# Kernel tuning notes

Hardware: AMD Instinct MI355X
Metric: run time of the kernel (lower is better)

The kernel has to match this reference:

```python
import jax, jax.numpy as jnp
import numpy as np

N_SEGMENT = 8  # frames per clip
N_DIV = 8      # fold divisor: fold = C // N_DIV channels shift each way


def setup_inputs() -> dict:
    key = jax.random.key(0)
    k1, k2 = jax.random.split(key)
    x = jax.random.normal(k1, (128, 256, 28, 28), dtype=jnp.float32)  # [nt, C, H, W], nt = 16 clips * 8 frames
    net_weight = jax.random.normal(k2, (256, 256), dtype=jnp.float32) * 0.0625  # 1x1 conv [out_c, in_c]
    return {"x": x, "net_weight": net_weight}


def temporal_shift(x):
    # x: [nt, C, H, W]. Equivalent to the fixed one-hot depthwise Conv3d (k=3, pad=1):
    #   channels [:fold]        -> out[t] = x[t-1]  (weight[...,0]=1)
    #   channels [fold:2*fold]  -> out[t] = x[t+1]  (weight[...,2]=1)
    #   channels [2*fold:]      -> out[t] = x[t]    (weight[...,1]=1)
    nt, c, h, w = x.shape
    b = nt // N_SEGMENT
    xv = x.reshape(b, N_SEGMENT, c, h, w)
    fold = c // N_DIV
    prev = jnp.pad(xv[:, :-1, :fold], ((0, 0), (1, 0), (0, 0), (0, 0), (0, 0)))       # shift right in time
    nxt = jnp.pad(xv[:, 1:, fold:2 * fold], ((0, 0), (0, 1), (0, 0), (0, 0), (0, 0)))  # shift left in time
    shifted = jnp.concatenate([prev, nxt, xv[:, :, 2 * fold:]], axis=2)
    return shifted.reshape(nt, c, h, w)


def reference(x, net_weight):
    y = temporal_shift(x)
    # wrapped net: 1x1 Conv2d(256 -> 256, bias=False) == per-pixel GEMM
    out = jnp.einsum('nchw,oc->nohw', y, net_weight)
    return out
```

## Files before the change

kernel.cpp:

```cpp
#include <hip/hip_runtime.h>
#include <hip/hip_bf16.h>


#define CDIM 256
#define HWPX 784
#define FRST (CDIM * HWPX)
#define P_TILE 112
#define NPT  7
#define NWG  (128 * NPT * 2)
#define LROW 264

using bf16x8 = __attribute__((ext_vector_type(8))) short;
using bf16x4 = __attribute__((ext_vector_type(4))) short;
using f32x4  = __attribute__((ext_vector_type(4))) float;

static __device__ __forceinline__ unsigned int pk2(float lo, float hi) {
    union { __hip_bfloat162 h; unsigned int u; } cv;
    cv.h = __float22bfloat162_rn(make_float2(lo, hi));
    return cv.u;
}

__global__ void wconv(const float* __restrict__ w, unsigned short* __restrict__ wb) {
    const int i = (blockIdx.x * 256 + threadIdx.x) * 4;
    f32x4 v = *(const f32x4*)(w + i);
    *(uint2*)(wb + i) = make_uint2(pk2(v[0], v[1]), pk2(v[2], v[3]));
}

__global__ __launch_bounds__(256, 2)
void tsm_ksplit(const float* __restrict__ x,
                const unsigned short* __restrict__ wb,
                float* __restrict__ out) {
    __shared__ __align__(16) unsigned short y[P_TILE * LROW];

    const int bid = blockIdx.x;
    const int wg  = (bid & 7) * (NWG / 8) + (bid >> 3);
    const int h    = wg & 1;
    const int pair = wg >> 1;
    const int n    = pair / NPT;
    const int pt   = pair - n * NPT;
    const int p0   = pt * P_TILE;
    const int tid  = threadIdx.x;
    const int tf   = n & 7;

    const int lane = tid & 63;
    const int wv   = tid >> 6;
    const int g    = lane >> 4;
    const int ol   = lane & 15;

    bf16x8 wf[8][2];
    #pragma unroll
    for (int kk = 0; kk < 8; ++kk)
        #pragma unroll
        for (int m = 0; m < 2; ++m) {
            const unsigned short* wp =
                &wb[(size_t)(h * 128 + wv * 32 + m * 16 + ol) * CDIM + kk * 32 + g * 8];
            asm volatile("global_load_dwordx4 %0, %1, off"
                         : "=v"(wf[kk][m]) : "v"(wp));
        }

    f32x4 r0[14], r1[14];
    #pragma unroll
    for (int i = 0; i < 14; ++i) {
        const int idx = tid + i * 256;
        const int cp  = idx / 28;
        const int pv  = idx - cp * 28;
        const int c0  = cp * 2;
        const int d   = (cp < 16) ? -1 : (cp < 32 ? 1 : 0);
        const bool valid = !((d == -1 && tf == 0) || (d == 1 && tf == 7));
        const float* s = x + ((size_t)(n + (valid ? d : 0)) * CDIM + c0) * HWPX
                           + p0 + pv * 4;
        asm volatile("global_load_dwordx4 %0, %1, off" : "=v"(r0[i]) : "v"(s));
        const float* s1 = s + HWPX;
        asm volatile("global_load_dwordx4 %0, %1, off" : "=v"(r1[i]) : "v"(s1));
    }

    #define WRITE_ITEM(i)                                                      \
    {                                                                          \
        const int idx = tid + (i) * 256;                                       \
        const int cp  = idx / 28;                                              \
        const int pv  = idx - cp * 28;                                         \
        const int c0  = cp * 2;                                                \
        const int d   = (cp < 16) ? -1 : (cp < 32 ? 1 : 0);                    \
        const bool valid = !((d == -1 && tf == 0) || (d == 1 && tf == 7));     \
        const int cc  = c0 ^ (((pv >> 1) & 7) << 2);       \
        const int rb  = pv * 4 * LROW + cc;                                    \
        _Pragma("unroll")                                                      \
        for (int r = 0; r < 4; ++r)                                            \
            *(unsigned int*)&y[rb + r * LROW] =                                \
                valid ? pk2(r0[i][r], r1[i][r]) : 0u;                          \
    }

    asm volatile("s_waitcnt vmcnt(14)" ::: "memory");
    __builtin_amdgcn_sched_barrier(0);
    #pragma unroll
    for (int i = 0; i < 7; ++i) WRITE_ITEM(i)
    __syncthreads();

    f32x4 acc[2][7];
    #pragma unroll
    for (int m = 0; m < 2; ++m)
        #pragma unroll
        for (int nn = 0; nn < 7; ++nn)
            acc[m][nn] = f32x4{0.f, 0.f, 0.f, 0.f};

    #define COMPUTE(K0, K1)                                                    \
    {                                                                          \
        _Pragma("unroll")                                                      \
        for (int nn = 0; nn < 7; ++nn) {                                       \
            const int p    = nn * 16 + ol;                                     \
            const int zz   = ((p >> 3) & 7) << 2;                              \
            const int rowb = p * LROW;                                         \
            _Pragma("unroll")                                                  \
            for (int kk = (K0); kk < (K1); ++kk) {                             \
                const int c  = kk * 32 + g * 8;                                \
                const int e0 = c ^ zz;                                         \
                const bf16x4 lo = *(const bf16x4*)&y[rowb + e0];               \
                const bf16x4 hi = *(const bf16x4*)&y[rowb + (e0 ^ 4)];         \
                const bf16x8 bf = __builtin_shufflevector(lo, hi,              \
                                                          0, 1, 2, 3, 4, 5, 6, 7); \
                acc[0][nn] = __builtin_amdgcn_mfma_f32_16x16x32_bf16(          \
                    wf[kk][0], bf, acc[0][nn], 0, 0, 0);                       \
                acc[1][nn] = __builtin_amdgcn_mfma_f32_16x16x32_bf16(          \
                    wf[kk][1], bf, acc[1][nn], 0, 0, 0);                       \
            }                                                                  \
        }                                                                      \
    }

    COMPUTE(0, 4)

    asm volatile("s_waitcnt vmcnt(0)" ::: "memory");
    __builtin_amdgcn_sched_barrier(0);
    #pragma unroll
    for (int i = 7; i < 14; ++i) WRITE_ITEM(i)
    __syncthreads();

    COMPUTE(4, 8)

    const size_t outbase = (size_t)n * CDIM * HWPX + p0 + ol;
    #pragma unroll
    for (int m = 0; m < 2; ++m) {
        #pragma unroll
        for (int r = 0; r < 4; ++r) {
            const int o = h * 128 + wv * 32 + m * 16 + g * 4 + r;
            float* orow = out + outbase + (size_t)o * HWPX;
            #pragma unroll
            for (int nn = 0; nn < 7; ++nn)
                orow[nn * 16] = acc[m][nn][r];
        }
    }
    #undef WRITE_ITEM
    #undef COMPUTE
}

#define LDS_STRIDE 264
__global__ __launch_bounds__(512, 4)
void tsm_fallback(const float* __restrict__ x, const float* __restrict__ w,
                  float* __restrict__ out) {
    __shared__ __align__(16) unsigned short ylds[P_TILE * LDS_STRIDE];
    const int n = blockIdx.x, tile = blockIdx.y, p0 = tile * P_TILE;
    const int tid = threadIdx.x, tf = n & 7;
    f32x4 v0[7], v1[7]; int cps[7], pvs[7];
    #pragma unroll
    for (int i = 0; i < 7; ++i) {
        const int idx = tid + i * 512, cp = idx / 28, pv = idx - cp * 28;
        cps[i] = cp; pvs[i] = pv;
        const int c0 = cp * 2;
        int nsrc; bool valid;
        if (c0 < 32)      { nsrc = n - 1; valid = (tf > 0); }
        else if (c0 < 64) { nsrc = n + 1; valid = (tf < 7); }
        else              { nsrc = n;     valid = true; }
        const float* src = x + ((size_t)(valid ? nsrc : n) * CDIM + c0) * HWPX + p0 + pv * 4;
        f32x4 a = {0,0,0,0}, b = {0,0,0,0};
        if (valid) { a = *(const f32x4*)src; b = *(const f32x4*)(src + HWPX); }
        v0[i] = a; v1[i] = b;
    }
    #pragma unroll
    for (int i = 0; i < 7; ++i) {
        const int c0 = cps[i] * 2, pv = pvs[i];
        const int cc = c0 ^ ((pv & 7) << 3);
        const int rb = pv * 4 * LDS_STRIDE + cc;
        #pragma unroll
        for (int r = 0; r < 4; ++r)
            *(unsigned int*)&ylds[rb + r * LDS_STRIDE] = pk2(v0[i][r], v1[i][r]);
    }
    __syncthreads();
    const int lane = tid & 63, wv = tid >> 6, g = lane >> 4, ol = lane & 15;
    f32x4 acc[2][7];
    #pragma unroll
    for (int m = 0; m < 2; ++m)
        #pragma unroll
        for (int nn = 0; nn < 7; ++nn) acc[m][nn] = f32x4{0,0,0,0};
    #pragma unroll
    for (int kk = 0; kk < 8; ++kk) {
        const int c = kk * 32 + g * 8;
        bf16x8 af[2];
        #pragma unroll
        for (int m = 0; m < 2; ++m) {
            const float* wp = w + (size_t)(wv * 32 + m * 16 + ol) * CDIM + c;
            f32x4 w0 = *(const f32x4*)wp, w1 = *(const f32x4*)(wp + 4);
            union { bf16x8 v; unsigned int u4[4]; } cv;
            cv.u4[0] = pk2(w0[0], w0[1]); cv.u4[1] = pk2(w0[2], w0[3]);
            cv.u4[2] = pk2(w1[0], w1[1]); cv.u4[3] = pk2(w1[2], w1[3]);
            af[m] = cv.v;
        }
        #pragma unroll
        for (int nn = 0; nn < 7; ++nn) {
            const int p = nn * 16 + ol;
            const int cc = c ^ (((p >> 2) & 7) << 3);
            const bf16x8 bf = *(const bf16x8*)&ylds[p * LDS_STRIDE + cc];
            #pragma unroll
            for (int m = 0; m < 2; ++m)
                acc[m][nn] = __builtin_amdgcn_mfma_f32_16x16x32_bf16(af[m], bf, acc[m][nn], 0, 0, 0);
        }
    }
    const size_t outbase = (size_t)n * CDIM * HWPX + p0 + ol;
    #pragma unroll
    for (int m = 0; m < 2; ++m)
        #pragma unroll
        for (int r = 0; r < 4; ++r) {
            const int o = wv * 32 + m * 16 + g * 4 + r;
            float* orow = out + outbase + (size_t)o * HWPX;
            #pragma unroll
            for (int nn = 0; nn < 7; ++nn) orow[nn * 16] = acc[m][nn][r];
        }
}

extern "C" void kernel_launch(void* const* d_in, const int* in_sizes, int n_in,
                              void* d_out, int out_size, void* d_ws, size_t ws_size,
                              hipStream_t stream) {
    const float* x = (const float*)d_in[0];
    const float* w = (const float*)d_in[1];
    float* out     = (float*)d_out;
    const size_t wb_bytes = (size_t)CDIM * CDIM * sizeof(unsigned short);
    if (ws_size >= wb_bytes) {
        unsigned short* wbuf = (unsigned short*)d_ws;
        wconv<<<64, 256, 0, stream>>>(w, wbuf);
        tsm_ksplit<<<NWG, 256, 0, stream>>>(x, wbuf, out);
    } else {
        tsm_fallback<<<dim3(128, 7, 1), dim3(512, 1, 1), 0, stream>>>(x, w, out);
    }
}
```

Before: 48.59 us.

## Process two frames per workgroup and prefetch the second frame during compute

Each workgroup now handles frame n1 and frame n1+64, which share the same temporal position and therefore the same shift pattern. The grid is halved. The bf16 weight fragments held in registers are reused across both frames, and the second frame's input loads are issued while the first frame's MFMAs and output stores run. The aim is to amortise the weight loads and launch cost and to hide global load latency. The costs are more register pressure, a longer per-workgroup critical path, and fewer workgroups (1.75 waves), which may worsen tail balance on an already bandwidth-heavy kernel.

```diff
diff --git a/kernel.cpp b/kernel.cpp
--- a/kernel.cpp
+++ b/kernel.cpp
@@ -7,7 +7,7 @@
 #define FRST (CDIM * HWPX)
 #define P_TILE 112
 #define NPT  7
-#define NWG  (128 * NPT * 2)
+#define NWGB 896
 #define LROW 264
 
 using bf16x8 = __attribute__((ext_vector_type(8))) short;
@@ -27,20 +27,21 @@
 }
 
 __global__ __launch_bounds__(256, 2)
-void tsm_ksplit(const float* __restrict__ x,
-                const unsigned short* __restrict__ wb,
-                float* __restrict__ out) {
+void tsm_pair(const float* __restrict__ x,
+              const unsigned short* __restrict__ wb,
+              float* __restrict__ out) {
     __shared__ __align__(16) unsigned short y[P_TILE * LROW];
 
-    const int bid = blockIdx.x;
-    const int wg  = (bid & 7) * (NWG / 8) + (bid >> 3);
+    const int bid  = blockIdx.x;
+    const int wg   = (bid & 7) * (NWGB / 8) + (bid >> 3);
     const int h    = wg & 1;
     const int pair = wg >> 1;
-    const int n    = pair / NPT;
-    const int pt   = pair - n * NPT;
+    const int n1   = pair / NPT;
+    const int pt   = pair - n1 * NPT;
     const int p0   = pt * P_TILE;
+    const int n2   = n1 + 64;
     const int tid  = threadIdx.x;
-    const int tf   = n & 7;
+    const int tf   = n1 & 7;
 
     const int lane = tid & 63;
     const int wv   = tid >> 6;
@@ -59,19 +60,21 @@
         }
 
     f32x4 r0[14], r1[14];
-    #pragma unroll
-    for (int i = 0; i < 14; ++i) {
-        const int idx = tid + i * 256;
-        const int cp  = idx / 28;
-        const int pv  = idx - cp * 28;
-        const int c0  = cp * 2;
-        const int d   = (cp < 16) ? -1 : (cp < 32 ? 1 : 0);
-        const bool valid = !((d == -1 && tf == 0) || (d == 1 && tf == 7));
-        const float* s = x + ((size_t)(n + (valid ? d : 0)) * CDIM + c0) * HWPX
-                           + p0 + pv * 4;
-        asm volatile("global_load_dwordx4 %0, %1, off" : "=v"(r0[i]) : "v"(s));
-        const float* s1 = s + HWPX;
-        asm volatile("global_load_dwordx4 %0, %1, off" : "=v"(r1[i]) : "v"(s1));
+    f32x4 acc[2][7];
+
+    #define ISSUE(i, N_)                                                       \
+    {                                                                          \
+        const int idx = tid + (i) * 256;                                       \
+        const int cp  = idx / 28;                                              \
+        const int pv  = idx - cp * 28;                                         \
+        const int c0  = cp * 2;                                                \
+        const int d   = (cp < 16) ? -1 : (cp < 32 ? 1 : 0);                    \
+        const bool valid = !((d == -1 && tf == 0) || (d == 1 && tf == 7));     \
+        const float* s = x + ((size_t)((N_) + (valid ? d : 0)) * CDIM + c0) * HWPX \
+                           + p0 + pv * 4;                                      \
+        asm volatile("global_load_dwordx4 %0, %1, off" : "=v"(r0[i]) : "v"(s));\
+        const float* s1 = s + HWPX;                                            \
+        asm volatile("global_load_dwordx4 %0, %1, off" : "=v"(r1[i]) : "v"(s1));\
     }
 
     #define WRITE_ITEM(i)                                                      \
@@ -90,18 +93,14 @@
                 valid ? pk2(r0[i][r], r1[i][r]) : 0u;                          \
     }
 
-    asm volatile("s_waitcnt vmcnt(14)" ::: "memory");
-    __builtin_amdgcn_sched_barrier(0);
-    #pragma unroll
-    for (int i = 0; i < 7; ++i) WRITE_ITEM(i)
-    __syncthreads();
-
-    f32x4 acc[2][7];
-    #pragma unroll
-    for (int m = 0; m < 2; ++m)
-        #pragma unroll
-        for (int nn = 0; nn < 7; ++nn)
-            acc[m][nn] = f32x4{0.f, 0.f, 0.f, 0.f};
+    #define ZERO_ACC                                                           \
+    {                                                                          \
+        _Pragma("unroll")                                                      \
+        for (int m = 0; m < 2; ++m)                                            \
+            _Pragma("unroll")                                                  \
+            for (int nn = 0; nn < 7; ++nn)                                     \
+                acc[m][nn] = f32x4{0.f, 0.f, 0.f, 0.f};                        \
+    }
 
     #define COMPUTE(K0, K1)                                                    \
     {                                                                          \
@@ -126,6 +125,32 @@
         }                                                                      \
     }
 
+    #define STORES(N_)                                                         \
+    {                                                                          \
+        const size_t outbase = (size_t)(N_) * CDIM * HWPX + p0 + ol;           \
+        _Pragma("unroll")                                                      \
+        for (int m = 0; m < 2; ++m) {                                          \
+            _Pragma("unroll")                                                  \
+            for (int r = 0; r < 4; ++r) {                                      \
+                const int o = h * 128 + wv * 32 + m * 16 + g * 4 + r;          \
+                float* orow = out + outbase + (size_t)o * HWPX;                \
+                _Pragma("unroll")                                              \
+                for (int nn = 0; nn < 7; ++nn)                                 \
+                    orow[nn * 16] = acc[m][nn][r];                             \
+            }                                                                  \
+        }                                                                      \
+    }
+
+    #pragma unroll
+    for (int i = 0; i < 14; ++i) ISSUE(i, n1)
+
+    asm volatile("s_waitcnt vmcnt(14)" ::: "memory");
+    __builtin_amdgcn_sched_barrier(0);
+    #pragma unroll
+    for (int i = 0; i < 7; ++i) WRITE_ITEM(i)
+    __syncthreads();
+
+    ZERO_ACC
     COMPUTE(0, 4)
 
     asm volatile("s_waitcnt vmcnt(0)" ::: "memory");
@@ -134,22 +159,37 @@
     for (int i = 7; i < 14; ++i) WRITE_ITEM(i)
     __syncthreads();
 
+    #pragma unroll
+    for (int i = 0; i < 7; ++i) ISSUE(i, n2)
     COMPUTE(4, 8)
-
-    const size_t outbase = (size_t)n * CDIM * HWPX + p0 + ol;
-    #pragma unroll
-    for (int m = 0; m < 2; ++m) {
-        #pragma unroll
-        for (int r = 0; r < 4; ++r) {
-            const int o = h * 128 + wv * 32 + m * 16 + g * 4 + r;
-            float* orow = out + outbase + (size_t)o * HWPX;
-            #pragma unroll
-            for (int nn = 0; nn < 7; ++nn)
-                orow[nn * 16] = acc[m][nn][r];
-        }
-    }
+    STORES(n1)
+
+    __syncthreads();
+    asm volatile("s_waitcnt vmcnt(56)" ::: "memory");
+    __builtin_amdgcn_sched_barrier(0);
+    #pragma unroll
+    for (int i = 0; i < 7; ++i) WRITE_ITEM(i)
+    __syncthreads();
+
+    ZERO_ACC
+    #pragma unroll
+    for (int i = 7; i < 14; ++i) ISSUE(i, n2)
+    COMPUTE(0, 4)
+
+    asm volatile("s_waitcnt vmcnt(0)" ::: "memory");
+    __builtin_amdgcn_sched_barrier(0);
+    #pragma unroll
+    for (int i = 7; i < 14; ++i) WRITE_ITEM(i)
+    __syncthreads();
+
+    COMPUTE(4, 8)
+    STORES(n2)
+
+    #undef ISSUE
     #undef WRITE_ITEM
+    #undef ZERO_ACC
     #undef COMPUTE
+    #undef STORES
 }
 
 #define LDS_STRIDE 264
@@ -235,7 +275,7 @@
     if (ws_size >= wb_bytes) {
         unsigned short* wbuf = (unsigned short*)d_ws;
         wconv<<<64, 256, 0, stream>>>(w, wbuf);
-        tsm_ksplit<<<NWG, 256, 0, stream>>>(x, wbuf, out);
+        tsm_pair<<<NWGB, 256, 0, stream>>>(x, wbuf, out);
     } else {
         tsm_fallback<<<dim3(128, 7, 1), dim3(512, 1, 1), 0, stream>>>(x, w, out);
     }
```

Result: slower. 102.8 us (+111.7%).

## Replace output-half split with full-output 64-pixel tiles and streamed weights

Applied to the files above, without the earlier changes.

Each workgroup now computes all 256 output channels for a flat 64-pixel tile that may cross frame boundaries, instead of half the outputs for a 112-pixel tile. Before, every input tile was loaded and converted twice, once per output half. Now each input is read once, and the weights are streamed in two K passes of 16 registers each. The cost is more weight-load traffic per pixel, smaller tiles, and per-element frame index division.

```diff
diff --git a/kernel.cpp b/kernel.cpp
--- a/kernel.cpp
+++ b/kernel.cpp
@@ -5,9 +5,8 @@
 #define CDIM 256
 #define HWPX 784
 #define FRST (CDIM * HWPX)
-#define P_TILE 112
-#define NPT  7
-#define NWG  (128 * NPT * 2)
+#define TPX  64
+#define NTILES 1568
 #define LROW 264
 
 using bf16x8 = __attribute__((ext_vector_type(8))) short;
@@ -27,60 +26,65 @@
 }
 
 __global__ __launch_bounds__(256, 2)
-void tsm_ksplit(const float* __restrict__ x,
-                const unsigned short* __restrict__ wb,
-                float* __restrict__ out) {
-    __shared__ __align__(16) unsigned short y[P_TILE * LROW];
+void tsm_full(const float* __restrict__ x,
+              const unsigned short* __restrict__ wb,
+              float* __restrict__ out) {
+    __shared__ __align__(16) unsigned short y[TPX * LROW];
 
     const int bid = blockIdx.x;
-    const int wg  = (bid & 7) * (NWG / 8) + (bid >> 3);
-    const int h    = wg & 1;
-    const int pair = wg >> 1;
-    const int n    = pair / NPT;
-    const int pt   = pair - n * NPT;
-    const int p0   = pt * P_TILE;
-    const int tid  = threadIdx.x;
-    const int tf   = n & 7;
-
+    const int t   = (bid & 7) * (NTILES / 8) + (bid >> 3);
+    const int tid = threadIdx.x;
     const int lane = tid & 63;
     const int wv   = tid >> 6;
     const int g    = lane >> 4;
     const int ol   = lane & 15;
 
-    bf16x8 wf[8][2];
-    #pragma unroll
-    for (int kk = 0; kk < 8; ++kk)
-        #pragma unroll
-        for (int m = 0; m < 2; ++m) {
-            const unsigned short* wp =
-                &wb[(size_t)(h * 128 + wv * 32 + m * 16 + ol) * CDIM + kk * 32 + g * 8];
-            asm volatile("global_load_dwordx4 %0, %1, off"
-                         : "=v"(wf[kk][m]) : "v"(wp));
-        }
-
-    f32x4 r0[14], r1[14];
-    #pragma unroll
-    for (int i = 0; i < 14; ++i) {
-        const int idx = tid + i * 256;
-        const int cp  = idx / 28;
-        const int pv  = idx - cp * 28;
-        const int c0  = cp * 2;
-        const int d   = (cp < 16) ? -1 : (cp < 32 ? 1 : 0);
-        const bool valid = !((d == -1 && tf == 0) || (d == 1 && tf == 7));
-        const float* s = x + ((size_t)(n + (valid ? d : 0)) * CDIM + c0) * HWPX
-                           + p0 + pv * 4;
-        asm volatile("global_load_dwordx4 %0, %1, off" : "=v"(r0[i]) : "v"(s));
-        const float* s1 = s + HWPX;
-        asm volatile("global_load_dwordx4 %0, %1, off" : "=v"(r1[i]) : "v"(s1));
-    }
-
-    #define WRITE_ITEM(i)                                                      \
+    bf16x8 wf[4][4];
+    f32x4  r0[8], r1[8];
+    f32x4  acc[4][4];
+
+    #define WISSUE(PASS)                                                       \
+    {                                                                          \
+        _Pragma("unroll")                                                      \
+        for (int kkh = 0; kkh < 4; ++kkh)                                      \
+            _Pragma("unroll")                                                  \
+            for (int m = 0; m < 4; ++m) {                                      \
+                const unsigned short* wp_ = wb +                               \
+                    (size_t)(wv * 64 + m * 16 + ol) * CDIM +                   \
+                    ((PASS) * 4 + kkh) * 32 + g * 8;                           \
+                asm volatile("global_load_dwordx4 %0, %1, off"                 \
+                             : "=v"(wf[kkh][m]) : "v"(wp_));                   \
+            }                                                                  \
+    }
+
+    #define ISSUE(i)                                                           \
     {                                                                          \
         const int idx = tid + (i) * 256;                                       \
-        const int cp  = idx / 28;                                              \
-        const int pv  = idx - cp * 28;                                         \
+        const int cp  = idx >> 4;                                              \
+        const int pv  = idx & 15;                                              \
         const int c0  = cp * 2;                                                \
         const int d   = (cp < 16) ? -1 : (cp < 32 ? 1 : 0);                    \
+        const int gq  = t * TPX + pv * 4;                                      \
+        const int nf  = gq / HWPX;                                             \
+        const int pin = gq - nf * HWPX;                                        \
+        const int tf  = nf & 7;                                                \
+        const bool valid = !((d == -1 && tf == 0) || (d == 1 && tf == 7));     \
+        const float* s = x + ((size_t)(nf + (valid ? d : 0)) * CDIM + c0) * HWPX + pin; \
+        asm volatile("global_load_dwordx4 %0, %1, off" : "=v"(r0[i]) : "v"(s));\
+        const float* s1 = s + HWPX;                                            \
+        asm volatile("global_load_dwordx4 %0, %1, off" : "=v"(r1[i]) : "v"(s1));\
+    }
+
+    #define WRITE_ITEM(i)                                                      \
+    {                                                                          \
+        const int idx = tid + (i) * 256;                                       \
+        const int cp  = idx >> 4;                                              \
+        const int pv  = idx & 15;                                              \
+        const int c0  = cp * 2;                                                \
+        const int d   = (cp < 16) ? -1 : (cp < 32 ? 1 : 0);                    \
+        const int gq  = t * TPX + pv * 4;                                      \
+        const int nf  = gq / HWPX;                                             \
+        const int tf  = nf & 7;                                                \
         const bool valid = !((d == -1 && tf == 0) || (d == 1 && tf == 7));     \
         const int cc  = c0 ^ (((pv >> 1) & 7) << 2);       \
         const int rb  = pv * 4 * LROW + cc;                                    \
@@ -90,68 +94,79 @@
                 valid ? pk2(r0[i][r], r1[i][r]) : 0u;                          \
     }
 
-    asm volatile("s_waitcnt vmcnt(14)" ::: "memory");
-    __builtin_amdgcn_sched_barrier(0);
-    #pragma unroll
-    for (int i = 0; i < 7; ++i) WRITE_ITEM(i)
-    __syncthreads();
-
-    f32x4 acc[2][7];
-    #pragma unroll
-    for (int m = 0; m < 2; ++m)
-        #pragma unroll
-        for (int nn = 0; nn < 7; ++nn)
-            acc[m][nn] = f32x4{0.f, 0.f, 0.f, 0.f};
-
-    #define COMPUTE(K0, K1)                                                    \
+    #define COMPUTE(PASS)                                                      \
     {                                                                          \
         _Pragma("unroll")                                                      \
-        for (int nn = 0; nn < 7; ++nn) {                                       \
-            const int p    = nn * 16 + ol;                                     \
-            const int zz   = ((p >> 3) & 7) << 2;                              \
-            const int rowb = p * LROW;                                         \
+        for (int nn = 0; nn < 4; ++nn) {                                       \
+            const int lp   = nn * 16 + ol;                                     \
+            const int zz   = ((lp >> 3) & 7) << 2;                             \
+            const int rowb = lp * LROW;                                        \
             _Pragma("unroll")                                                  \
-            for (int kk = (K0); kk < (K1); ++kk) {                             \
-                const int c  = kk * 32 + g * 8;                                \
+            for (int kkh = 0; kkh < 4; ++kkh) {                                \
+                const int c  = ((PASS) * 4 + kkh) * 32 + g * 8;                \
                 const int e0 = c ^ zz;                                         \
                 const bf16x4 lo = *(const bf16x4*)&y[rowb + e0];               \
                 const bf16x4 hi = *(const bf16x4*)&y[rowb + (e0 ^ 4)];         \
                 const bf16x8 bf = __builtin_shufflevector(lo, hi,              \
                                                           0, 1, 2, 3, 4, 5, 6, 7); \
-                acc[0][nn] = __builtin_amdgcn_mfma_f32_16x16x32_bf16(          \
-                    wf[kk][0], bf, acc[0][nn], 0, 0, 0);                       \
-                acc[1][nn] = __builtin_amdgcn_mfma_f32_16x16x32_bf16(          \
-                    wf[kk][1], bf, acc[1][nn], 0, 0, 0);                       \
+                _Pragma("unroll")                                              \
+                for (int m = 0; m < 4; ++m)                                    \
+                    acc[m][nn] = __builtin_amdgcn_mfma_f32_16x16x32_bf16(      \
+                        wf[kkh][m], bf, acc[m][nn], 0, 0, 0);                  \
             }                                                                  \
         }                                                                      \
     }
 
-    COMPUTE(0, 4)
+    WISSUE(0)
+    #pragma unroll
+    for (int i = 0; i < 8; ++i) ISSUE(i)
+
+    asm volatile("s_waitcnt vmcnt(8)" ::: "memory");
+    __builtin_amdgcn_sched_barrier(0);
+    #pragma unroll
+    for (int i = 0; i < 4; ++i) WRITE_ITEM(i)
+    __syncthreads();
+
+    #pragma unroll
+    for (int m = 0; m < 4; ++m)
+        #pragma unroll
+        for (int nn = 0; nn < 4; ++nn)
+            acc[m][nn] = f32x4{0.f, 0.f, 0.f, 0.f};
+
+    COMPUTE(0)
+
+    WISSUE(1)
+    asm volatile("s_waitcnt vmcnt(16)" ::: "memory");
+    __builtin_amdgcn_sched_barrier(0);
+    #pragma unroll
+    for (int i = 4; i < 8; ++i) WRITE_ITEM(i)
+    __syncthreads();
 
     asm volatile("s_waitcnt vmcnt(0)" ::: "memory");
     __builtin_amdgcn_sched_barrier(0);
-    #pragma unroll
-    for (int i = 7; i < 14; ++i) WRITE_ITEM(i)
-    __syncthreads();
-
-    COMPUTE(4, 8)
-
-    const size_t outbase = (size_t)n * CDIM * HWPX + p0 + ol;
-    #pragma unroll
-    for (int m = 0; m < 2; ++m) {
-        #pragma unroll
-        for (int r = 0; r < 4; ++r) {
-            const int o = h * 128 + wv * 32 + m * 16 + g * 4 + r;
-            float* orow = out + outbase + (size_t)o * HWPX;
+
+    COMPUTE(1)
+
+    #pragma unroll
+    for (int nn = 0; nn < 4; ++nn) {
+        const int gq  = t * TPX + nn * 16 + ol;
+        const int nf  = gq / HWPX;
+        const int pin = gq - nf * HWPX;
+        float* ob = out + (size_t)nf * FRST + pin;
+        #pragma unroll
+        for (int m = 0; m < 4; ++m)
             #pragma unroll
-            for (int nn = 0; nn < 7; ++nn)
-                orow[nn * 16] = acc[m][nn][r];
-        }
-    }
+            for (int r = 0; r < 4; ++r)
+                ob[(size_t)(wv * 64 + m * 16 + g * 4 + r) * HWPX] = acc[m][nn][r];
+    }
+
+    #undef WISSUE
+    #undef ISSUE
     #undef WRITE_ITEM
     #undef COMPUTE
 }
 
+#define P_TILE 112
 #define LDS_STRIDE 264
 __global__ __launch_bounds__(512, 4)
 void tsm_fallback(const float* __restrict__ x, const float* __restrict__ w,
@@ -235,7 +250,7 @@
     if (ws_size >= wb_bytes) {
         unsigned short* wbuf = (unsigned short*)d_ws;
         wconv<<<64, 256, 0, stream>>>(w, wbuf);
-        tsm_ksplit<<<NWG, 256, 0, stream>>>(x, wbuf, out);
+        tsm_full<<<NTILES, 256, 0, stream>>>(x, wbuf, out);
     } else {
         tsm_fallback<<<dim3(128, 7, 1), dim3(512, 1, 1), 0, stream>>>(x, w, out);
     }
```

After: 61.65 us. 1.27x slower.
